# Performance work log

Hardware: AMD Instinct MI355X
Metric: run time of the kernel (lower is better)

The kernel has to match this reference:

```python
import jax, jax.numpy as jnp
import numpy as np

S, B, D, DV = 2048, 16, 128, 128


def setup_inputs() -> dict:
    key = jax.random.key(0)
    kq, kk, kv = jax.random.split(key, 3)
    return {
        "query": jax.random.normal(kq, (S, B, D), dtype=jnp.float32),
        "key": jax.random.normal(kk, (S, B, D), dtype=jnp.float32),
        "value": jax.random.normal(kv, (S, B, DV), dtype=jnp.float32),
    }


def reference(query, key, value):
    # sim: [B, S_q, S_k]
    d = key.shape[-1]
    sim = jnp.einsum('sbd,tbd->bst', query, key) / jnp.sqrt(jnp.asarray(d, query.dtype))
    # causal mask: disallow attending to future positions (strictly upper triangle)
    sq, sk = sim.shape[-2], sim.shape[-1]
    causal = jnp.tril(jnp.ones((sq, sk), dtype=bool))  # [S_q, S_k]
    sim = jnp.where(causal[None, :, :], sim, -jnp.inf)
    a = jax.nn.softmax(sim, axis=-1)  # dropout omitted (eval mode, p=0)
    # context: [S_q, B, D_v]
    context = jnp.einsum('bst,tbe->sbe', a, value)
    return context
```

## Files before the change

### kernel.cpp

```cpp
#include <hip/hip_runtime.h>
#include <stdint.h>

#define SS 2048
#define BB 16
#define DD 128
#define DVV 128
#define BQ 32
#define BK 32
#define NTILES (SS / BK)
#define TILE_HW 4096

typedef __attribute__((ext_vector_type(8))) short short8;
typedef __attribute__((ext_vector_type(4))) float float4v;

__device__ __forceinline__ short f2bf(float f) {
  union { float f; uint32_t u; } x;
  x.f = f;
  uint32_t r = x.u + 0x7fffu + ((x.u >> 16) & 1u);
  return (short)(r >> 16);
}

__device__ __forceinline__ int kappa(int quad, int j) {
  return (j < 4) ? (quad * 4 + j) : (16 + quad * 4 + (j - 4));
}

__global__ __launch_bounds__(256) void conv_kv(
    const float* __restrict__ kg, const float* __restrict__ vg,
    short* __restrict__ kimg, short* __restrict__ vimg) {
  __shared__ short tile[BK][136];
  const int t = blockIdx.x, b = blockIdx.y;
  const float* src_base = (blockIdx.z == 0) ? kg : vg;
  short* out = ((blockIdx.z == 0) ? kimg : vimg) + ((size_t)(b * NTILES + t)) * TILE_HW;
#pragma unroll
  for (int p = 0; p < 2; ++p) {
    const int ch = threadIdx.x + p * 256;
    const int key = ch >> 4, c = ch & 15;
    const float* src = src_base + ((size_t)(t * BK + key) * BB + b) * DD + c * 8;
    float4v f0 = *(const float4v*)src;
    float4v f1 = *(const float4v*)(src + 4);
    short8 s;
#pragma unroll
    for (int i = 0; i < 4; ++i) { s[i] = f2bf(f0[i]); s[4 + i] = f2bf(f1[i]); }
    *(short8*)&tile[key][c * 8] = s;
  }
  __syncthreads();
#pragma unroll
  for (int p = 0; p < 2; ++p) {
    const int idx = threadIdx.x + p * 256;
    const int j = idx >> 6, quad = (idx >> 4) & 3, mm = idx & 15;
    short8 s;
    if (blockIdx.z == 0) {
      const int ks = j >> 1, half = j & 1;
      s = *(const short8*)&tile[half * 16 + mm][(ks * 4 + quad) * 8];
    } else {
#pragma unroll
      for (int jj = 0; jj < 8; ++jj) s[jj] = tile[kappa(quad, jj)][j * 16 + mm];
    }
    *(short8*)(out + idx * 8) = s;
  }
}

__global__ __launch_bounds__(256, 4) void attn_fwd(
    const float* __restrict__ qg, const short* __restrict__ kimg,
    const short* __restrict__ vimg, float* __restrict__ og) {
  __shared__ __align__(16) float cw[128 * 36];

  const int tid   = threadIdx.x;
  const int wave  = tid >> 6;
  const int qwave = wave & 1;
  const int tpar  = wave >> 1;
  const int lane  = tid & 63;
  const int m     = lane & 15;
  const int quad  = lane >> 4;
  const int bid   = blockIdx.x;
  const int g  = (bid >> 4) & 15;
  const int ph = bid >> 8;
  const int b  = ((bid & 7) << 1) | ((bid >> 3) & 1);
  const int qt = (ph == 0) ? 63 - g : (ph == 1) ? g : (ph == 2) ? 47 - g : 16 + g;
  const int qw = qt * BQ + qwave * 16;
  const int qrow = qw + m;

  const float cscale = 0.08838834764831845f * 1.4426950408889634f;
  short8 qfrag[4];
#pragma unroll
  for (int ks = 0; ks < 4; ++ks) {
    const float* qp = qg + ((size_t)qrow * BB + b) * DD + ks * 32 + quad * 8;
    float4v f0 = *(const float4v*)qp;
    float4v f1 = *(const float4v*)(qp + 4);
    short8 f;
#pragma unroll
    for (int i = 0; i < 4; ++i) { f[i] = f2bf(f0[i] * cscale); f[4 + i] = f2bf(f1[i] * cscale); }
    qfrag[ks] = f;
  }

  float4v oacc[8];
#pragma unroll
  for (int i = 0; i < 8; ++i) oacc[i] = (float4v){0.f, 0.f, 0.f, 0.f};
  float psum = 0.f;

  const short* kt = kimg + (size_t)b * NTILES * TILE_HW + lane * 8;
  const short* vt = vimg + (size_t)b * NTILES * TILE_HW + lane * 8;
  const int ntile = qt + 1;

  for (int t = tpar; t < ntile; t += 2) {
    const short* kp = kt + (size_t)t * TILE_HW;
    const short* vp = vt + (size_t)t * TILE_HW;

    float4v s0 = {0.f, 0.f, 0.f, 0.f}, s1 = {0.f, 0.f, 0.f, 0.f};
#pragma unroll
    for (int ks = 0; ks < 4; ++ks) {
      short8 kf0 = *(const short8*)(kp + (ks * 2 + 0) * 512);
      short8 kf1 = *(const short8*)(kp + (ks * 2 + 1) * 512);
      s0 = __builtin_amdgcn_mfma_f32_16x16x32_bf16(kf0, qfrag[ks], s0, 0, 0, 0);
      s1 = __builtin_amdgcn_mfma_f32_16x16x32_bf16(kf1, qfrag[ks], s1, 0, 0, 0);
    }
    float sv[8];
#pragma unroll
    for (int rr = 0; rr < 4; ++rr) { sv[rr] = s0[rr]; sv[4 + rr] = s1[rr]; }

    const int kt0 = t * BK;
    if (kt0 + BK - 1 > qw) {
#pragma unroll
      for (int j = 0; j < 8; ++j)
        if (kt0 + kappa(quad, j) > qrow) sv[j] = -1e30f;
    }

    union { short8 s8; uint32_t w[4]; } pf;
#pragma unroll
    for (int jp = 0; jp < 4; ++jp) {
      float p0 = exp2f(sv[2 * jp]);
      float p1 = exp2f(sv[2 * jp + 1]);
      uint32_t w;
      asm("v_cvt_pk_bf16_f32 %0, %1, %2" : "=v"(w) : "v"(p0), "v"(p1));
      pf.w[jp] = w;
      union { uint32_t u; float f; } lo, hi;
      lo.u = w << 16;
      hi.u = w & 0xffff0000u;
      psum += lo.f;
      psum += hi.f;
    }
    const short8 pfrag = pf.s8;

#pragma unroll
    for (int nt = 0; nt < 8; ++nt) {
      short8 vf = *(const short8*)(vp + nt * 512);
      oacc[nt] = __builtin_amdgcn_mfma_f32_16x16x32_bf16(pfrag, vf, oacc[nt], 0, 0, 0);
    }
  }

  if (tpar == 1) {
    float* p = cw + (size_t)(qwave * 64 + lane) * 36;
#pragma unroll
    for (int nt = 0; nt < 8; ++nt) *(float4v*)(p + nt * 4) = oacc[nt];
    p[32] = psum;
  }
  __syncthreads();
  if (tpar == 0) {
    const float* p = cw + (size_t)(qwave * 64 + lane) * 36;
#pragma unroll
    for (int nt = 0; nt < 8; ++nt) oacc[nt] += *(const float4v*)(p + nt * 4);
    psum += p[32];

    float l = psum;
    l += __shfl_xor(l, 16, 64);
    l += __shfl_xor(l, 32, 64);
    const float linv = 1.0f / l;
    float l4[4];
#pragma unroll
    for (int rr = 0; rr < 4; ++rr) l4[rr] = __shfl(linv, quad * 4 + rr, 64);
#pragma unroll
    for (int rr = 0; rr < 4; ++rr) {
      const int qgl = qw + quad * 4 + rr;
      float* op = og + ((size_t)qgl * BB + b) * DVV + m;
#pragma unroll
      for (int nt = 0; nt < 8; ++nt) op[nt * 16] = oacc[nt][rr] * l4[rr];
    }
  }
}

extern "C" void kernel_launch(void* const* d_in, const int* in_sizes, int n_in,
                              void* d_out, int out_size, void* d_ws, size_t ws_size,
                              hipStream_t stream) {
  const float* q = (const float*)d_in[0];
  const float* k = (const float*)d_in[1];
  const float* v = (const float*)d_in[2];
  float* out = (float*)d_out;
  short* kimg = (short*)d_ws;
  short* vimg = kimg + (size_t)BB * NTILES * TILE_HW;

  conv_kv<<<dim3(NTILES, BB, 2), 256, 0, stream>>>(k, v, kimg, vimg);
  attn_fwd<<<dim3(SS / BQ * BB), 256, 0, stream>>>(q, kimg, vimg, out);
}
```

Baseline: 144.4 us.

## Share K/V tiles across four query waves via LDS direct loads

Raises the query block to 64 rows, giving four waves with 16 rows each, all iterating over every key tile. Each tile's K and V images are staged once into LDS with global_load_lds, replacing the per-wave global loads. The two-way key-split partial reduction through LDS is removed. This cuts global/L2 traffic by sharing tiles across waves, but adds two block barriers per tile with no double buffering, and halves the number of blocks.

```diff
diff --git a/kernel.cpp b/kernel.cpp
--- a/kernel.cpp
+++ b/kernel.cpp
@@ -5,13 +5,16 @@
 #define BB 16
 #define DD 128
 #define DVV 128
-#define BQ 32
+#define BQ 64
 #define BK 32
 #define NTILES (SS / BK)
 #define TILE_HW 4096
 
 typedef __attribute__((ext_vector_type(8))) short short8;
 typedef __attribute__((ext_vector_type(4))) float float4v;
+
+typedef __attribute__((address_space(1))) const void glob_cv;
+typedef __attribute__((address_space(3))) void lds_v;
 
 __device__ __forceinline__ short f2bf(float f) {
   union { float f; uint32_t u; } x;
@@ -60,24 +63,22 @@
   }
 }
 
-__global__ __launch_bounds__(256, 4) void attn_fwd(
+__global__ __launch_bounds__(256) void attn_fwd(
     const float* __restrict__ qg, const short* __restrict__ kimg,
     const short* __restrict__ vimg, float* __restrict__ og) {
-  __shared__ __align__(16) float cw[128 * 36];
+  __shared__ __align__(16) short smem[16 * 512];
 
-  const int tid   = threadIdx.x;
-  const int wave  = tid >> 6;
-  const int qwave = wave & 1;
-  const int tpar  = wave >> 1;
-  const int lane  = tid & 63;
-  const int m     = lane & 15;
-  const int quad  = lane >> 4;
-  const int bid   = blockIdx.x;
-  const int g  = (bid >> 4) & 15;
-  const int ph = bid >> 8;
-  const int b  = ((bid & 7) << 1) | ((bid >> 3) & 1);
-  const int qt = (ph == 0) ? 63 - g : (ph == 1) ? g : (ph == 2) ? 47 - g : 16 + g;
-  const int qw = qt * BQ + qwave * 16;
+  const int tid  = threadIdx.x;
+  const int wave = tid >> 6;
+  const int lane = tid & 63;
+  const int m    = lane & 15;
+  const int quad = lane >> 4;
+  const int bid  = blockIdx.x;
+  const int xcd = bid & 7;
+  const int j   = bid >> 3;
+  const int qt  = (j < 32) ? j : 63 - j;
+  const int b   = 2 * xcd + (j >> 5);
+  const int qw  = qt * BQ + wave * 16;
   const int qrow = qw + m;
 
   const float cscale = 0.08838834764831845f * 1.4426950408889634f;
@@ -98,19 +99,33 @@
   for (int i = 0; i < 8; ++i) oacc[i] = (float4v){0.f, 0.f, 0.f, 0.f};
   float psum = 0.f;
 
-  const short* kt = kimg + (size_t)b * NTILES * TILE_HW + lane * 8;
-  const short* vt = vimg + (size_t)b * NTILES * TILE_HW + lane * 8;
-  const int ntile = qt + 1;
+  const short* kbase = kimg + (size_t)b * NTILES * TILE_HW;
+  const short* vbase = vimg + (size_t)b * NTILES * TILE_HW;
+  const int cbase = wave * 4;
+  const short* timg = (cbase < 8) ? kbase : vbase;
+  const int coff = cbase & 7;
 
-  for (int t = tpar; t < ntile; t += 2) {
-    const short* kp = kt + (size_t)t * TILE_HW;
-    const short* vp = vt + (size_t)t * TILE_HW;
+  const int ntile = 2 * qt + 2;
+
+  for (int r = 0; r < ntile; ++r) {
+    __syncthreads();
+    {
+      const short* src = timg + (size_t)r * TILE_HW + coff * 512 + lane * 8;
+#pragma unroll
+      for (int c = 0; c < 4; ++c)
+        __builtin_amdgcn_global_load_lds((glob_cv*)(src + c * 512),
+                                         (lds_v*)&smem[(cbase + c) * 512], 16, 0, 0);
+    }
+    __syncthreads();
+
+    const short* kb = smem;
+    const short* vb = smem + 8 * 512;
 
     float4v s0 = {0.f, 0.f, 0.f, 0.f}, s1 = {0.f, 0.f, 0.f, 0.f};
 #pragma unroll
     for (int ks = 0; ks < 4; ++ks) {
-      short8 kf0 = *(const short8*)(kp + (ks * 2 + 0) * 512);
-      short8 kf1 = *(const short8*)(kp + (ks * 2 + 1) * 512);
+      short8 kf0 = *(const short8*)(kb + (ks * 2 + 0) * 512 + lane * 8);
+      short8 kf1 = *(const short8*)(kb + (ks * 2 + 1) * 512 + lane * 8);
       s0 = __builtin_amdgcn_mfma_f32_16x16x32_bf16(kf0, qfrag[ks], s0, 0, 0, 0);
       s1 = __builtin_amdgcn_mfma_f32_16x16x32_bf16(kf1, qfrag[ks], s1, 0, 0, 0);
     }
@@ -118,11 +133,11 @@
 #pragma unroll
     for (int rr = 0; rr < 4; ++rr) { sv[rr] = s0[rr]; sv[4 + rr] = s1[rr]; }
 
-    const int kt0 = t * BK;
+    const int kt0 = r * BK;
     if (kt0 + BK - 1 > qw) {
 #pragma unroll
-      for (int j = 0; j < 8; ++j)
-        if (kt0 + kappa(quad, j) > qrow) sv[j] = -1e30f;
+      for (int jj = 0; jj < 8; ++jj)
+        if (kt0 + kappa(quad, jj) > qrow) sv[jj] = -1e30f;
     }
 
     union { short8 s8; uint32_t w[4]; } pf;
@@ -143,38 +158,24 @@
 
 #pragma unroll
     for (int nt = 0; nt < 8; ++nt) {
-      short8 vf = *(const short8*)(vp + nt * 512);
+      short8 vf = *(const short8*)(vb + nt * 512 + lane * 8);
       oacc[nt] = __builtin_amdgcn_mfma_f32_16x16x32_bf16(pfrag, vf, oacc[nt], 0, 0, 0);
     }
   }
 
-  if (tpar == 1) {
-    float* p = cw + (size_t)(qwave * 64 + lane) * 36;
+  float l = psum;
+  l += __shfl_xor(l, 16, 64);
+  l += __shfl_xor(l, 32, 64);
+  const float linv = 1.0f / l;
+  float l4[4];
 #pragma unroll
-    for (int nt = 0; nt < 8; ++nt) *(float4v*)(p + nt * 4) = oacc[nt];
-    p[32] = psum;
-  }
-  __syncthreads();
-  if (tpar == 0) {
-    const float* p = cw + (size_t)(qwave * 64 + lane) * 36;
+  for (int rr = 0; rr < 4; ++rr) l4[rr] = __shfl(linv, quad * 4 + rr, 64);
 #pragma unroll
-    for (int nt = 0; nt < 8; ++nt) oacc[nt] += *(const float4v*)(p + nt * 4);
-    psum += p[32];
-
-    float l = psum;
-    l += __shfl_xor(l, 16, 64);
-    l += __shfl_xor(l, 32, 64);
-    const float linv = 1.0f / l;
-    float l4[4];
+  for (int rr = 0; rr < 4; ++rr) {
+    const int qgl = qw + quad * 4 + rr;
+    float* op = og + ((size_t)qgl * BB + b) * DVV + m;
 #pragma unroll
-    for (int rr = 0; rr < 4; ++rr) l4[rr] = __shfl(linv, quad * 4 + rr, 64);
-#pragma unroll
-    for (int rr = 0; rr < 4; ++rr) {
-      const int qgl = qw + quad * 4 + rr;
-      float* op = og + ((size_t)qgl * BB + b) * DVV + m;
-#pragma unroll
-      for (int nt = 0; nt < 8; ++nt) op[nt * 16] = oacc[nt][rr] * l4[rr];
-    }
+    for (int nt = 0; nt < 8; ++nt) op[nt * 16] = oacc[nt][rr] * l4[rr];
   }
 }
 
```

Result: no change. 146.8 us (+1.6%).
